# Kernel tuning notes

Hardware: AMD Instinct MI355X
Metric: run time of the kernel (lower is better)

## Reference

```python
import jax, jax.numpy as jnp
import numpy as np

K = 6

def _diag_indices(H, W):
    # stable argsort of anti-diagonal index i+j over row-major flattening
    i = np.arange(H)[:, None]
    j = np.arange(W)[None, :]
    order = np.argsort((i + j).ravel(), kind='stable')
    return order, np.argsort(order, kind='stable')

def _selective_scan(u, delta, A, Bs, Cs, D, delta_bias):
    # u, delta: (B,K,D,L); A: (K,D,N); Bs,Cs: (B,K,N,L); D,delta_bias: (K,D)
    delta = jax.nn.softplus(delta + delta_bias[None, :, :, None])
    dA = jnp.exp(jnp.einsum('bkdl,kdn->lbkdn', delta, A))          # (L,B,K,D,N)
    dBu = jnp.einsum('bkdl,bknl,bkdl->lbkdn', delta, Bs, u)         # (L,B,K,D,N)
    Cl = jnp.moveaxis(Cs, -1, 0)                                    # (L,B,K,N)
    x0 = jnp.zeros(dA.shape[1:], dA.dtype)
    def step(x, inp):
        dA_t, dBu_t, C_t = inp
        x = dA_t * x + dBu_t
        y = jnp.einsum('bkdn,bkn->bkd', x, C_t)
        return x, y
    _, ys = jax.lax.scan(step, x0, (dA, dBu, Cl))
    y = jnp.moveaxis(ys, 0, -1)                                     # (B,K,D,L)
    return y + u * D[None, :, :, None]

def reference(x, W_in, conv_w, conv_b, x_proj_w, dt_w, dt_b, A_logs, Ds, ln_g, ln_b, W_out):
    B, H, W, C = x.shape
    L = H * W
    di = dt_w.shape[1]
    dt_rank = dt_w.shape[2]
    N = A_logs.shape[1]
    # in_proj (no bias) and split
    xz = jnp.einsum('bhwc,oc->bhwo', x, W_in)
    xx, z = jnp.split(xz, 2, axis=-1)
    # depthwise conv 3x3, SAME padding, + bias, SiLU
    xc = jnp.transpose(xx, (0, 3, 1, 2))                            # (B,di,H,W)
    xc = jax.lax.conv_general_dilated(xc, conv_w, (1, 1), 'SAME',
            feature_group_count=di, dimension_numbers=('NCHW', 'OIHW', 'NCHW'))
    xc = jax.nn.silu(xc + conv_b[None, :, None, None])
    # build 6 scan orderings
    x_flat = xc.reshape(B, di, L)
    x_t = jnp.transpose(xc, (0, 1, 3, 2)).reshape(B, di, L)
    x_hwwh = jnp.stack([x_flat, x_t], axis=1)                       # (B,2,di,L)
    xs4 = jnp.concatenate([x_hwwh, x_hwwh[..., ::-1]], axis=1)      # (B,4,di,L)
    x_invhh = jnp.flip(xc, axis=-1).reshape(B, di, L)               # flip W only
    x_hh = jnp.stack([x_flat, x_invhh], axis=1)                     # (B,2,di,L)
    diag_idx, rev_idx = _diag_indices(H, W)
    xs = jnp.concatenate([xs4, x_hh[..., diag_idx]], axis=1)        # (B,6,di,L)
    # projections
    x_dbl = jnp.einsum('bkdl,kcd->bkcl', xs, x_proj_w)
    dts, Bs, Cs = jnp.split(x_dbl, [dt_rank, dt_rank + N], axis=2)
    dts = jnp.einsum('bkrl,kdr->bkdl', dts, dt_w)
    A = -jnp.exp(A_logs).reshape(K, di, N)
    out_y = _selective_scan(xs, dts, A, Bs, Cs, Ds.reshape(K, di), dt_b)
    # undo the 6 orderings
    inv_y = out_y[:, 2:4][..., ::-1]
    wh_y = jnp.transpose(out_y[:, 1].reshape(B, di, W, H), (0, 1, 3, 2)).reshape(B, di, L)
    invwh_y = jnp.transpose(inv_y[:, 1].reshape(B, di, W, H), (0, 1, 3, 2)).reshape(B, di, L)
    transhh = out_y[:, 4:6][..., rev_idx]
    invhh = transhh[:, 1][..., ::-1]
    y = out_y[:, 0] + inv_y[:, 0] + wh_y + invwh_y + transhh[:, 0] + invhh  # (B,di,L)
    y = jnp.transpose(y, (0, 2, 1)).reshape(B, H, W, di)
    # LayerNorm (eps=1e-5)
    mu = y.mean(-1, keepdims=True)
    var = ((y - mu) ** 2).mean(-1, keepdims=True)
    y = (y - mu) * jax.lax.rsqrt(var + 1e-5) * ln_g + ln_b
    y = y * jax.nn.silu(z)
    return jnp.einsum('bhwd,od->bhwo', y, W_out)

def setup_inputs():
    key = jax.random.key(0)
    ks = jax.random.split(key, 8)
    d_model, di, N, dt_rank = 64, 128, 16, 4
    x = jax.random.normal(ks[0], (1, 64, 64, d_model), jnp.float32)
    W_in = jax.random.normal(ks[1], (2 * di, d_model), jnp.float32) * d_model ** -0.5
    conv_w = jax.random.normal(ks[2], (di, 1, 3, 3), jnp.float32) / 3.0
    conv_b = jnp.zeros((di,), jnp.float32)
    x_proj_w = jax.random.normal(ks[3], (K, dt_rank + 2 * N, di), jnp.float32) * di ** -0.5
    s = dt_rank ** -0.5
    dt_w = jax.random.uniform(ks[4], (K, di, dt_rank), jnp.float32, -s, s)
    dt = jnp.exp(jax.random.uniform(ks[5], (K, di), jnp.float32)
                 * (np.log(0.1) - np.log(0.001)) + np.log(0.001))
    dt = jnp.clip(dt, 1e-4)
    dt_b = dt + jnp.log(-jnp.expm1(-dt))
    A_logs = jnp.log(jnp.tile(jnp.arange(1, N + 1, dtype=jnp.float32)[None, :], (K * di, 1)))
    Ds = jnp.ones((K * di,), jnp.float32)
    ln_g = jnp.ones((di,), jnp.float32)
    ln_b = jnp.zeros((di,), jnp.float32)
    W_out = jax.random.normal(ks[6], (d_model, di), jnp.float32) * di ** -0.5
    return {"x": x, "W_in": W_in, "conv_w": conv_w, "conv_b": conv_b,
            "x_proj_w": x_proj_w, "dt_w": dt_w, "dt_b": dt_b, "A_logs": A_logs,
            "Ds": Ds, "ln_g": ln_g, "ln_b": ln_b, "W_out": W_out}
```

## Files before the change

### kernel.cpp

```cpp
#include <hip/hip_runtime.h>
#include <math.h>

#define L    4096
#define DI   128
#define NS   16
#define KK   6
#define CM   64
#define NC   256
#define CH   16

__device__ __forceinline__ float softplus_f(float x){
    return x > 20.f ? x : __logf(1.f + __expf(x));
}
__device__ __forceinline__ float silu_f(float x){
    return x / (1.f + __expf(-x));
}

__device__ __forceinline__ int rankp(int p){
    int h = p >> 6, w = p & 63, s = h + w;
    int imin = s > 63 ? s - 63 : 0;
    int off = (s < 64) ? (s*(s+1))/2 : 4096 - ((127-s)*(128-s))/2;
    return off + (h - imin);
}

__device__ __forceinline__ int perm_in(int k, int l, const int* __restrict__ diag){
    switch(k){
        case 0: return l;
        case 1: return ((l&63)<<6) | (l>>6);
        case 2: return (L-1) - l;
        case 3: { int m = (L-1)-l; return ((m&63)<<6) | (m>>6); }
        case 4: return diag[l];
        default: return diag[l] ^ 63;
    }
}

__global__ __launch_bounds__(256) void k_init(const float* __restrict__ W_in,
                                              const float* __restrict__ W_out,
                                              const float* __restrict__ conv_w,
                                              const float* __restrict__ xpw,
                                              int* __restrict__ diag_idx,
                                              float* __restrict__ WI4,
                                              float* __restrict__ WO4,
                                              float* __restrict__ cwT,
                                              float* __restrict__ PW40){
    int t = blockIdx.x*256 + threadIdx.x;
    diag_idx[rankp(t)] = t;
    {
        int d4 = t >> 8, o = t & 255;
        ((float4*)WI4)[d4*256 + o] = make_float4(
            W_in[(size_t)o*CM + d4*4+0], W_in[(size_t)o*CM + d4*4+1],
            W_in[(size_t)o*CM + d4*4+2], W_in[(size_t)o*CM + d4*4+3]);
    }
    if(t < 2048){
        int d4 = t >> 6, o = t & 63;
        ((float4*)WO4)[d4*64 + o] = make_float4(
            W_out[(size_t)o*DI + d4*4+0], W_out[(size_t)o*DI + d4*4+1],
            W_out[(size_t)o*DI + d4*4+2], W_out[(size_t)o*DI + d4*4+3]);
    }
    if(t < 9*DI){
        int tap = t >> 7, d = t & 127;
        cwT[t] = conv_w[d*9 + tap];
    }
    for(int r = t; r < KK*40*32; r += 4096){
        int k = r / (40*32), rem = r % (40*32);
        int c = rem >> 5, dd4 = rem & 31;
        float4 v = make_float4(0.f, 0.f, 0.f, 0.f);
        if(c < 36) v = ((const float4*)(xpw + ((size_t)k*36 + c)*DI))[dd4];
        ((float4*)PW40)[r] = v;
    }
}

__global__ __launch_bounds__(256) void k_inproj(const float* __restrict__ x,
                                                const float* __restrict__ WI4,
                                                float* __restrict__ xx_t,
                                                float* __restrict__ sz){
    int pb = blockIdx.x * 8;
    int o  = threadIdx.x;
    __shared__ float xr[8][CM];
    if(o < 128) ((float4*)&xr[0][0])[o] = ((const float4*)(x + (size_t)pb*CM))[o];
    float4 w[16];
    const float4* W4 = (const float4*)WI4;
    #pragma unroll
    for(int q=0;q<16;q++) w[q] = W4[q*256 + o];
    __syncthreads();
    float acc[8];
    #pragma unroll
    for(int pi=0;pi<8;pi++) acc[pi] = 0.f;
    #pragma unroll
    for(int q=0;q<16;q++){
        float4 wv = w[q];
        #pragma unroll
        for(int pi=0;pi<8;pi++){
            float4 xv = *((const float4*)&xr[pi][q*4]);
            acc[pi] += wv.x*xv.x + wv.y*xv.y + wv.z*xv.z + wv.w*xv.w;
        }
    }
    #pragma unroll
    for(int pi=0;pi<8;pi++){
        int p = pb + pi;
        if(o < DI) xx_t[(size_t)p*DI + o] = acc[pi];
        else       sz[(size_t)p*DI + (o-DI)] = silu_f(acc[pi]);
    }
}

__global__ __launch_bounds__(256) void k_conv(const float* __restrict__ xx_t,
                                              const float* __restrict__ cwT,
                                              const float* __restrict__ cb,
                                              float* __restrict__ xc_t){
    int idx = blockIdx.x*256 + threadIdx.x;
    int dq = (idx & 31)*4, p = idx >> 5;
    int h = p >> 6, w = p & 63;
    float4 acc = *((const float4*)(cb + dq));
    #pragma unroll
    for(int dh=-1; dh<=1; dh++){
        int hh = h+dh; if(hh < 0 || hh >= 64) continue;
        #pragma unroll
        for(int dw=-1; dw<=1; dw++){
            int ww = w+dw; if(ww < 0 || ww >= 64) continue;
            int tap = (dh+1)*3 + (dw+1);
            float4 xv = *((const float4*)(xx_t + (size_t)(hh*64+ww)*DI + dq));
            float4 wv = *((const float4*)(cwT + tap*DI + dq));
            acc.x += wv.x*xv.x; acc.y += wv.y*xv.y;
            acc.z += wv.z*xv.z; acc.w += wv.w*xv.w;
        }
    }
    *((float4*)(xc_t + (size_t)p*DI + dq)) =
        make_float4(silu_f(acc.x), silu_f(acc.y), silu_f(acc.z), silu_f(acc.w));
}

#define XT_S 132
__global__ __launch_bounds__(256) void k_projscan(const float* __restrict__ xc_t,
                                                  const float* __restrict__ PW40,
                                                  const int* __restrict__ diag,
                                                  const float* __restrict__ dtw,
                                                  const float* __restrict__ dtb,
                                                  const float* __restrict__ A_logs,
                                                  float* __restrict__ dts,
                                                  float* __restrict__ BT,
                                                  float* __restrict__ CT,
                                                  float* __restrict__ apb,
                                                  float* __restrict__ xlb){
    int b = blockIdx.x;
    int k = b % KK, tile = b / KK;
    int l0 = tile * 32;
    int t = threadIdx.x;
    __shared__ float xt[32*XT_S];
    __shared__ float Btl[32*NS];
    __shared__ float dtt[4*32];

    #pragma unroll
    for(int q=0;q<4;q++){
        int lin = q*256 + t;
        int row = lin >> 5, col4 = lin & 31;
        int p = perm_in(k, l0+row, diag);
        float4 v = ((const float4*)(xc_t + (size_t)p*DI))[col4];
        *((float4*)(xt + row*XT_S + col4*4)) = v;
    }
    __syncthreads();

    {
        int l = t & 31, g = t >> 5;
        const float* xr = xt + l*XT_S;
        float acc[5];
        #pragma unroll
        for(int j=0;j<5;j++) acc[j] = 0.f;
        const float4* wbase = (const float4*)PW40 + (size_t)k*40*32;
        for(int dd4=0; dd4<32; dd4++){
            float4 xv = *((const float4*)(xr + dd4*4));
            #pragma unroll
            for(int j=0;j<5;j++){
                float4 wv = wbase[(g*5+j)*32 + dd4];
                acc[j] += wv.x*xv.x + wv.y*xv.y + wv.z*xv.z + wv.w*xv.w;
            }
        }
        #pragma unroll
        for(int j=0;j<5;j++){
            int c = g*5 + j;
            if(c < 4){
                dts[((size_t)k*4 + c)*L + l0 + l] = acc[j];
                dtt[c*32 + l] = acc[j];
            } else if(c < 20){
                BT[((size_t)k*L + l0 + l)*NS + (c-4)] = acc[j];
                Btl[l*NS + (c-4)] = acc[j];
            } else if(c < 36){
                CT[((size_t)k*L + l0 + l)*NS + (c-20)] = acc[j];
            }
        }
    }
    __syncthreads();

    int h = t >> 7, d = t & 127;
    int cc = tile*2 + h;
    float4 w4 = ((const float4*)dtw)[(size_t)k*DI + d];
    float  bb = dtb[k*DI + d];
    float A[NS];
    {
        const float4* ar = (const float4*)(A_logs + ((size_t)k*DI + d)*NS);
        #pragma unroll
        for(int q=0;q<4;q++){
            float4 a4 = ar[q];
            A[q*4+0] = -__expf(a4.x); A[q*4+1] = -__expf(a4.y);
            A[q*4+2] = -__expf(a4.z); A[q*4+3] = -__expf(a4.w);
        }
    }
    float xs[NS], ap[NS];
    #pragma unroll
    for(int n=0;n<NS;n++){ xs[n] = 0.f; ap[n] = 1.f; }
    #pragma unroll
    for(int i=0;i<CH;i++){
        int l = h*CH + i;
        float u = xt[l*XT_S + d];
        float dv = bb + w4.x*dtt[l] + w4.y*dtt[32+l] + w4.z*dtt[64+l] + w4.w*dtt[96+l];
        float delta = softplus_f(dv);
        float du = delta*u;
        const float* Bi = Btl + l*NS;
        #pragma unroll
        for(int n=0;n<NS;n++){
            float da = __expf(delta*A[n]);
            xs[n] = da*xs[n] + du*Bi[n];
            ap[n] *= da;
        }
    }
    int bk = k*NC + cc;
    float* apd = apb + ((size_t)bk*DI + d)*NS;
    float* xld = xlb + ((size_t)bk*DI + d)*NS;
    #pragma unroll
    for(int q=0;q<4;q++){
        ((float4*)apd)[q] = make_float4(ap[q*4],ap[q*4+1],ap[q*4+2],ap[q*4+3]);
        ((float4*)xld)[q] = make_float4(xs[q*4],xs[q*4+1],xs[q*4+2],xs[q*4+3]);
    }
}

__global__ __launch_bounds__(512) void k_comb(float* __restrict__ apb,
                                              const float* __restrict__ xlb){
    int k    = blockIdx.x >> 5;
    int gidx = blockIdx.x & 31;
    int seg  = threadIdx.x >> 6;
    int c    = threadIdx.x & 63;
    int rem  = gidx*64 + c;
    size_t sb = (size_t)k*NC*2048 + (size_t)seg*32*2048 + rem;
    float a[32], xl[32];
    #pragma unroll
    for(int j=0;j<32;j++){
        a[j]  = apb[sb + (size_t)j*2048];
        xl[j] = xlb[sb + (size_t)j*2048];
    }
    float Aag = 1.f, Xag = 0.f;
    #pragma unroll
    for(int j=0;j<32;j++){ Xag = a[j]*Xag + xl[j]; Aag *= a[j]; }
    __shared__ float sA[64][8], sX[64][8];
    sA[c][seg] = Aag; sX[c][seg] = Xag;
    __syncthreads();
    if(threadIdx.x < 64){
        float run = 0.f;
        #pragma unroll
        for(int s=0;s<8;s++){
            float at = sA[c][s], xt = sX[c][s];
            sX[c][s] = run;
            run = at*run + xt;
        }
    }
    __syncthreads();
    float run = sX[c][seg];
    #pragma unroll
    for(int j=0;j<32;j++){
        apb[sb + (size_t)j*2048] = run;
        run = a[j]*run + xl[j];
    }
}

__global__ __launch_bounds__(128) void k_scan2(const float* __restrict__ xc_t,
                                               const float* __restrict__ dts,
                                               const float* __restrict__ BT,
                                               const float* __restrict__ CT,
                                               const float* __restrict__ dtw,
                                               const float* __restrict__ dtb,
                                               const float* __restrict__ A_logs,
                                               const float* __restrict__ Dsv,
                                               const int* __restrict__ diag,
                                               const float* __restrict__ inib,
                                               float* __restrict__ yk){
    int bk = blockIdx.x;
    int k = bk >> 8, cc = bk & (NC-1);
    int d = threadIdx.x;
    int l0 = cc*CH;
    __shared__ float Bt[CH*NS];
    __shared__ float Ct[CH*NS];
    __shared__ float dtt[4*CH];
    __shared__ int   pt[CH];
    if(d < 64){
        ((float4*)Bt)[d] = ((const float4*)(BT + ((size_t)k*L + l0)*NS))[d];
        int r = d>>4, i = d&15;
        dtt[d] = dts[((size_t)k*4 + r)*L + l0 + i];
    } else {
        ((float4*)Ct)[d-64] = ((const float4*)(CT + ((size_t)k*L + l0)*NS))[d-64];
    }
    if(d < CH) pt[d] = perm_in(k, l0+d, diag);
    __syncthreads();
    float u[CH];
    #pragma unroll
    for(int i=0;i<CH;i++) u[i] = xc_t[(size_t)pt[i]*DI + d];
    float4 w4 = ((const float4*)dtw)[(size_t)k*DI + d];
    float  bb = dtb[k*DI + d];
    float  Dv = Dsv[k*DI + d];
    float A[NS];
    {
        const float4* ar = (const float4*)(A_logs + ((size_t)k*DI + d)*NS);
        #pragma unroll
        for(int q=0;q<4;q++){
            float4 a4 = ar[q];
            A[q*4+0] = -__expf(a4.x); A[q*4+1] = -__expf(a4.y);
            A[q*4+2] = -__expf(a4.z); A[q*4+3] = -__expf(a4.w);
        }
    }
    float xv[NS];
    {
        const float4* ir = (const float4*)(inib + ((size_t)bk*DI + d)*NS);
        #pragma unroll
        for(int q=0;q<4;q++){
            float4 v = ir[q];
            xv[q*4+0]=v.x; xv[q*4+1]=v.y; xv[q*4+2]=v.z; xv[q*4+3]=v.w;
        }
    }
    #pragma unroll
    for(int i=0;i<CH;i++){
        float dv = bb + w4.x*dtt[i] + w4.y*dtt[CH+i] + w4.z*dtt[2*CH+i] + w4.w*dtt[3*CH+i];
        float delta = softplus_f(dv);
        float du = delta*u[i];
        const float* Bi = Bt + i*NS;
        const float* Ci = Ct + i*NS;
        float y = 0.f;
        #pragma unroll
        for(int n=0;n<NS;n++){
            float da = __expf(delta*A[n]);
            xv[n] = da*xv[n] + du*Bi[n];
            y += xv[n]*Ci[n];
        }
        yk[((size_t)k*L + l0 + i)*DI + d] = y + u[i]*Dv;
    }
}

__global__ __launch_bounds__(128) void k_out(const float* __restrict__ yk,
                                             const float* __restrict__ sz,
                                             const float* __restrict__ ln_g,
                                             const float* __restrict__ ln_b,
                                             const float* __restrict__ WO4,
                                             float* __restrict__ out){
    int pb = blockIdx.x*4;
    int d = threadIdx.x;
    __shared__ float ms[4][DI];
    __shared__ float red[4][2][2];
    float g = ln_g[d], bc = ln_b[d];
    float yv[4];
    #pragma unroll
    for(int pi=0;pi<4;pi++){
        int p = pb+pi;
        int tp = ((p&63)<<6) | (p>>6);
        float y;
        y  = yk[((size_t)0*L + p)*DI + d];
        y += yk[((size_t)1*L + tp)*DI + d];
        y += yk[((size_t)2*L + (L-1-p))*DI + d];
        y += yk[((size_t)3*L + (L-1-tp))*DI + d];
        y += yk[((size_t)4*L + rankp(p))*DI + d];
        y += yk[((size_t)5*L + rankp(L-1-p))*DI + d];
        yv[pi] = y;
        float s1 = y, s2 = y*y;
        #pragma unroll
        for(int m=1;m<64;m<<=1){ s1 += __shfl_xor(s1,m,64); s2 += __shfl_xor(s2,m,64); }
        if((d&63)==0){ red[pi][d>>6][0] = s1; red[pi][d>>6][1] = s2; }
    }
    __syncthreads();
    #pragma unroll
    for(int pi=0;pi<4;pi++){
        float mu  = (red[pi][0][0]+red[pi][1][0]) * (1.f/DI);
        float var = (red[pi][0][1]+red[pi][1][1]) * (1.f/DI) - mu*mu;
        float yh = (yv[pi]-mu)*rsqrtf(var+1e-5f)*g + bc;
        ms[pi][d] = yh * sz[(size_t)(pb+pi)*DI + d];
    }
    __syncthreads();
    int o = d & 63, w = d >> 6;
    const float4* W4 = (const float4*)WO4;
    float acc[2];
    acc[0] = 0.f; acc[1] = 0.f;
    #pragma unroll 8
    for(int d4=0; d4<32; d4++){
        float4 wv = W4[d4*64 + o];
        #pragma unroll
        for(int q=0;q<2;q++){
            float4 xv = *((const float4*)&ms[w*2+q][d4*4]);
            acc[q] += wv.x*xv.x + wv.y*xv.y + wv.z*xv.z + wv.w*xv.w;
        }
    }
    #pragma unroll
    for(int q=0;q<2;q++)
        out[(size_t)(pb + w*2 + q)*CM + o] = acc[q];
}

extern "C" void kernel_launch(void* const* d_in, const int* in_sizes, int n_in,
                              void* d_out, int out_size, void* d_ws, size_t ws_size,
                              hipStream_t stream) {
    const float* x      = (const float*)d_in[0];
    const float* W_in   = (const float*)d_in[1];
    const float* conv_w = (const float*)d_in[2];
    const float* conv_b = (const float*)d_in[3];
    const float* xpw    = (const float*)d_in[4];
    const float* dtw    = (const float*)d_in[5];
    const float* dtb    = (const float*)d_in[6];
    const float* A_logs = (const float*)d_in[7];
    const float* Dsv    = (const float*)d_in[8];
    const float* ln_g   = (const float*)d_in[9];
    const float* ln_b   = (const float*)d_in[10];
    const float* W_out  = (const float*)d_in[11];
    float* out = (float*)d_out;

    float* ws = (float*)d_ws;
    float* xx_t = ws;
    float* sz   = xx_t + (size_t)L*DI;
    float* xc_t = sz   + (size_t)L*DI;
    float* dts  = xc_t + (size_t)L*DI;
    float* BT   = dts  + (size_t)KK*4*L;
    float* CT   = BT   + (size_t)KK*L*NS;
    float* apb  = CT   + (size_t)KK*L*NS;
    float* xlb  = apb  + (size_t)KK*NC*DI*NS;
    float* yk   = xlb  + (size_t)KK*NC*DI*NS;
    int*   diag = (int*)(yk + (size_t)KK*L*DI);
    float* WI4  = (float*)(diag + L);
    float* WO4  = WI4 + (size_t)16*256*4;
    float* cwT  = WO4 + (size_t)32*64*4;
    float* PW40 = cwT + (size_t)9*DI;

    k_init    <<<L/256, 256, 0, stream>>>(W_in, W_out, conv_w, xpw, diag, WI4, WO4, cwT, PW40);
    k_inproj  <<<L/8, 256, 0, stream>>>(x, WI4, xx_t, sz);
    k_conv    <<<(L*DI/4)/256, 256, 0, stream>>>(xx_t, cwT, conv_b, xc_t);
    k_projscan<<<KK*128, 256, 0, stream>>>(xc_t, PW40, diag, dtw, dtb, A_logs,
                                           dts, BT, CT, apb, xlb);
    k_comb    <<<KK*32, 512, 0, stream>>>(apb, xlb);
    k_scan2   <<<KK*NC, 128, 0, stream>>>(xc_t, dts, BT, CT, dtw, dtb, A_logs, Dsv, diag, apb, yk);
    k_out     <<<L/4, 128, 0, stream>>>(yk, sz, ln_g, ln_b, WO4, out);
}
```

Baseline: 165.3 us.

## Drop init kernel by reading raw weights and computing diagonal permutation inline

Removes the k_init launch that built the diagonal index table and repacked the in-proj, out-proj, conv and x-proj weights. Kernels now read the original weight layouts directly, and the diagonal scan order is computed arithmetically with a sqrt-based inverse rank. Several kernels change shape along the way: the conv goes from float4 per thread to scalar, the x-proj splits its work as 5/4 rows per group with no padding, out-proj weights are held in registers, and k_comb uses more, smaller blocks. This saves a launch and its global traffic, at the cost of strided weight loads and extra ALU work for the inverse rank.

```diff
diff --git a/kernel.cpp b/kernel.cpp
--- a/kernel.cpp
+++ b/kernel.cpp
@@ -23,55 +23,38 @@
     return off + (h - imin);
 }
 
-__device__ __forceinline__ int perm_in(int k, int l, const int* __restrict__ diag){
+__device__ __forceinline__ int invrank(int r){
+    int s, i;
+    if(r < 2080){
+        s = (int)((sqrtf(8.f*(float)r + 1.f) - 1.f) * 0.5f);
+        while(((s+1)*(s+2))/2 <= r) s++;
+        while((s*(s+1))/2 > r) s--;
+        i = r - (s*(s+1))/2;
+    } else {
+        int q = 4096 - r;
+        int u = (int)((sqrtf(8.f*(float)q + 1.f) - 1.f) * 0.5f);
+        while((u*(u+1))/2 < q) u++;
+        while(u > 1 && ((u-1)*u)/2 >= q) u--;
+        s = 127 - u;
+        int off = 4096 - (u*(u+1))/2;
+        i = (s - 63) + (r - off);
+    }
+    return (i << 6) | (s - i);
+}
+
+__device__ __forceinline__ int perm_in(int k, int l){
     switch(k){
         case 0: return l;
         case 1: return ((l&63)<<6) | (l>>6);
         case 2: return (L-1) - l;
         case 3: { int m = (L-1)-l; return ((m&63)<<6) | (m>>6); }
-        case 4: return diag[l];
-        default: return diag[l] ^ 63;
-    }
-}
-
-__global__ __launch_bounds__(256) void k_init(const float* __restrict__ W_in,
-                                              const float* __restrict__ W_out,
-                                              const float* __restrict__ conv_w,
-                                              const float* __restrict__ xpw,
-                                              int* __restrict__ diag_idx,
-                                              float* __restrict__ WI4,
-                                              float* __restrict__ WO4,
-                                              float* __restrict__ cwT,
-                                              float* __restrict__ PW40){
-    int t = blockIdx.x*256 + threadIdx.x;
-    diag_idx[rankp(t)] = t;
-    {
-        int d4 = t >> 8, o = t & 255;
-        ((float4*)WI4)[d4*256 + o] = make_float4(
-            W_in[(size_t)o*CM + d4*4+0], W_in[(size_t)o*CM + d4*4+1],
-            W_in[(size_t)o*CM + d4*4+2], W_in[(size_t)o*CM + d4*4+3]);
-    }
-    if(t < 2048){
-        int d4 = t >> 6, o = t & 63;
-        ((float4*)WO4)[d4*64 + o] = make_float4(
-            W_out[(size_t)o*DI + d4*4+0], W_out[(size_t)o*DI + d4*4+1],
-            W_out[(size_t)o*DI + d4*4+2], W_out[(size_t)o*DI + d4*4+3]);
-    }
-    if(t < 9*DI){
-        int tap = t >> 7, d = t & 127;
-        cwT[t] = conv_w[d*9 + tap];
-    }
-    for(int r = t; r < KK*40*32; r += 4096){
-        int k = r / (40*32), rem = r % (40*32);
-        int c = rem >> 5, dd4 = rem & 31;
-        float4 v = make_float4(0.f, 0.f, 0.f, 0.f);
-        if(c < 36) v = ((const float4*)(xpw + ((size_t)k*36 + c)*DI))[dd4];
-        ((float4*)PW40)[r] = v;
+        case 4: return invrank(l);
+        default: return invrank(l) ^ 63;
     }
 }
 
 __global__ __launch_bounds__(256) void k_inproj(const float* __restrict__ x,
-                                                const float* __restrict__ WI4,
+                                                const float* __restrict__ W_in,
                                                 float* __restrict__ xx_t,
                                                 float* __restrict__ sz){
     int pb = blockIdx.x * 8;
@@ -79,9 +62,9 @@
     __shared__ float xr[8][CM];
     if(o < 128) ((float4*)&xr[0][0])[o] = ((const float4*)(x + (size_t)pb*CM))[o];
     float4 w[16];
-    const float4* W4 = (const float4*)WI4;
-    #pragma unroll
-    for(int q=0;q<16;q++) w[q] = W4[q*256 + o];
+    const float4* wrow = (const float4*)(W_in + (size_t)o*CM);
+    #pragma unroll
+    for(int q=0;q<16;q++) w[q] = wrow[q];
     __syncthreads();
     float acc[8];
     #pragma unroll
@@ -104,34 +87,28 @@
 }
 
 __global__ __launch_bounds__(256) void k_conv(const float* __restrict__ xx_t,
-                                              const float* __restrict__ cwT,
+                                              const float* __restrict__ cw,
                                               const float* __restrict__ cb,
                                               float* __restrict__ xc_t){
     int idx = blockIdx.x*256 + threadIdx.x;
-    int dq = (idx & 31)*4, p = idx >> 5;
+    int d = idx & 127, p = idx >> 7;
     int h = p >> 6, w = p & 63;
-    float4 acc = *((const float4*)(cb + dq));
+    float acc = cb[d];
     #pragma unroll
     for(int dh=-1; dh<=1; dh++){
         int hh = h+dh; if(hh < 0 || hh >= 64) continue;
         #pragma unroll
         for(int dw=-1; dw<=1; dw++){
             int ww = w+dw; if(ww < 0 || ww >= 64) continue;
-            int tap = (dh+1)*3 + (dw+1);
-            float4 xv = *((const float4*)(xx_t + (size_t)(hh*64+ww)*DI + dq));
-            float4 wv = *((const float4*)(cwT + tap*DI + dq));
-            acc.x += wv.x*xv.x; acc.y += wv.y*xv.y;
-            acc.z += wv.z*xv.z; acc.w += wv.w*xv.w;
-        }
-    }
-    *((float4*)(xc_t + (size_t)p*DI + dq)) =
-        make_float4(silu_f(acc.x), silu_f(acc.y), silu_f(acc.z), silu_f(acc.w));
+            acc += cw[d*9 + (dh+1)*3+(dw+1)] * xx_t[(size_t)(hh*64+ww)*DI + d];
+        }
+    }
+    xc_t[idx] = silu_f(acc);
 }
 
 #define XT_S 132
 __global__ __launch_bounds__(256) void k_projscan(const float* __restrict__ xc_t,
-                                                  const float* __restrict__ PW40,
-                                                  const int* __restrict__ diag,
+                                                  const float* __restrict__ xpw,
                                                   const float* __restrict__ dtw,
                                                   const float* __restrict__ dtb,
                                                   const float* __restrict__ A_logs,
@@ -152,7 +129,7 @@
     for(int q=0;q<4;q++){
         int lin = q*256 + t;
         int row = lin >> 5, col4 = lin & 31;
-        int p = perm_in(k, l0+row, diag);
+        int p = perm_in(k, l0+row);
         float4 v = ((const float4*)(xc_t + (size_t)p*DI))[col4];
         *((float4*)(xt + row*XT_S + col4*4)) = v;
     }
@@ -160,30 +137,36 @@
 
     {
         int l = t & 31, g = t >> 5;
+        int cbase = (g < 4) ? 5*g : 20 + 4*(g-4);
+        int cnt   = (g < 4) ? 5 : 4;
         const float* xr = xt + l*XT_S;
         float acc[5];
         #pragma unroll
         for(int j=0;j<5;j++) acc[j] = 0.f;
-        const float4* wbase = (const float4*)PW40 + (size_t)k*40*32;
+        const float4* wbase = (const float4*)(xpw + (size_t)k*36*DI);
         for(int dd4=0; dd4<32; dd4++){
             float4 xv = *((const float4*)(xr + dd4*4));
             #pragma unroll
             for(int j=0;j<5;j++){
-                float4 wv = wbase[(g*5+j)*32 + dd4];
-                acc[j] += wv.x*xv.x + wv.y*xv.y + wv.z*xv.z + wv.w*xv.w;
+                if(j < cnt){
+                    float4 wv = wbase[(cbase+j)*32 + dd4];
+                    acc[j] += wv.x*xv.x + wv.y*xv.y + wv.z*xv.z + wv.w*xv.w;
+                }
             }
         }
         #pragma unroll
         for(int j=0;j<5;j++){
-            int c = g*5 + j;
-            if(c < 4){
-                dts[((size_t)k*4 + c)*L + l0 + l] = acc[j];
-                dtt[c*32 + l] = acc[j];
-            } else if(c < 20){
-                BT[((size_t)k*L + l0 + l)*NS + (c-4)] = acc[j];
-                Btl[l*NS + (c-4)] = acc[j];
-            } else if(c < 36){
-                CT[((size_t)k*L + l0 + l)*NS + (c-20)] = acc[j];
+            if(j < cnt){
+                int c = cbase + j;
+                if(c < 4){
+                    dts[((size_t)k*4 + c)*L + l0 + l] = acc[j];
+                    dtt[c*32 + l] = acc[j];
+                } else if(c < 20){
+                    BT[((size_t)k*L + l0 + l)*NS + (c-4)] = acc[j];
+                    Btl[l*NS + (c-4)] = acc[j];
+                } else {
+                    CT[((size_t)k*L + l0 + l)*NS + (c-20)] = acc[j];
+                }
             }
         }
     }
@@ -231,39 +214,40 @@
     }
 }
 
-__global__ __launch_bounds__(512) void k_comb(float* __restrict__ apb,
+__global__ __launch_bounds__(256) void k_comb(float* __restrict__ apb,
                                               const float* __restrict__ xlb){
-    int k    = blockIdx.x >> 5;
-    int gidx = blockIdx.x & 31;
-    int seg  = threadIdx.x >> 6;
-    int c    = threadIdx.x & 63;
-    int rem  = gidx*64 + c;
-    size_t sb = (size_t)k*NC*2048 + (size_t)seg*32*2048 + rem;
-    float a[32], xl[32];
-    #pragma unroll
-    for(int j=0;j<32;j++){
+    int k    = blockIdx.x >> 7;
+    int gidx = blockIdx.x & 127;
+    int seg  = threadIdx.x >> 4;
+    int c    = threadIdx.x & 15;
+    int rem  = gidx*16 + c;
+    size_t sb = (size_t)k*NC*2048 + (size_t)seg*16*2048 + rem;
+    float a[16], xl[16];
+    #pragma unroll
+    for(int j=0;j<16;j++){
         a[j]  = apb[sb + (size_t)j*2048];
         xl[j] = xlb[sb + (size_t)j*2048];
     }
     float Aag = 1.f, Xag = 0.f;
     #pragma unroll
-    for(int j=0;j<32;j++){ Xag = a[j]*Xag + xl[j]; Aag *= a[j]; }
-    __shared__ float sA[64][8], sX[64][8];
+    for(int j=0;j<16;j++){ Xag = a[j]*Xag + xl[j]; Aag *= a[j]; }
+    __shared__ float sA[16][17], sX[16][17];
     sA[c][seg] = Aag; sX[c][seg] = Xag;
     __syncthreads();
-    if(threadIdx.x < 64){
+    if(threadIdx.x < 16){
+        int cc = threadIdx.x;
         float run = 0.f;
         #pragma unroll
-        for(int s=0;s<8;s++){
-            float at = sA[c][s], xt = sX[c][s];
-            sX[c][s] = run;
+        for(int s=0;s<16;s++){
+            float at = sA[cc][s], xt = sX[cc][s];
+            sX[cc][s] = run;
             run = at*run + xt;
         }
     }
     __syncthreads();
     float run = sX[c][seg];
     #pragma unroll
-    for(int j=0;j<32;j++){
+    for(int j=0;j<16;j++){
         apb[sb + (size_t)j*2048] = run;
         run = a[j]*run + xl[j];
     }
@@ -277,7 +261,6 @@
                                                const float* __restrict__ dtb,
                                                const float* __restrict__ A_logs,
                                                const float* __restrict__ Dsv,
-                                               const int* __restrict__ diag,
                                                const float* __restrict__ inib,
                                                float* __restrict__ yk){
     int bk = blockIdx.x;
@@ -295,7 +278,7 @@
     } else {
         ((float4*)Ct)[d-64] = ((const float4*)(CT + ((size_t)k*L + l0)*NS))[d-64];
     }
-    if(d < CH) pt[d] = perm_in(k, l0+d, diag);
+    if(d < CH) pt[d] = perm_in(k, l0+d);
     __syncthreads();
     float u[CH];
     #pragma unroll
@@ -344,7 +327,7 @@
                                              const float* __restrict__ sz,
                                              const float* __restrict__ ln_g,
                                              const float* __restrict__ ln_b,
-                                             const float* __restrict__ WO4,
+                                             const float* __restrict__ W_out,
                                              float* __restrict__ out){
     int pb = blockIdx.x*4;
     int d = threadIdx.x;
@@ -379,12 +362,15 @@
     }
     __syncthreads();
     int o = d & 63, w = d >> 6;
-    const float4* W4 = (const float4*)WO4;
+    float4 wreg[32];
+    const float4* wr4 = (const float4*)(W_out + (size_t)o*DI);
+    #pragma unroll
+    for(int q=0;q<32;q++) wreg[q] = wr4[q];
     float acc[2];
     acc[0] = 0.f; acc[1] = 0.f;
-    #pragma unroll 8
+    #pragma unroll
     for(int d4=0; d4<32; d4++){
-        float4 wv = W4[d4*64 + o];
+        float4 wv = wreg[d4];
         #pragma unroll
         for(int q=0;q<2;q++){
             float4 xv = *((const float4*)&ms[w*2+q][d4*4]);
@@ -423,18 +409,12 @@
     float* apb  = CT   + (size_t)KK*L*NS;
     float* xlb  = apb  + (size_t)KK*NC*DI*NS;
     float* yk   = xlb  + (size_t)KK*NC*DI*NS;
-    int*   diag = (int*)(yk + (size_t)KK*L*DI);
-    float* WI4  = (float*)(diag + L);
-    float* WO4  = WI4 + (size_t)16*256*4;
-    float* cwT  = WO4 + (size_t)32*64*4;
-    float* PW40 = cwT + (size_t)9*DI;
-
-    k_init    <<<L/256, 256, 0, stream>>>(W_in, W_out, conv_w, xpw, diag, WI4, WO4, cwT, PW40);
-    k_inproj  <<<L/8, 256, 0, stream>>>(x, WI4, xx_t, sz);
-    k_conv    <<<(L*DI/4)/256, 256, 0, stream>>>(xx_t, cwT, conv_b, xc_t);
-    k_projscan<<<KK*128, 256, 0, stream>>>(xc_t, PW40, diag, dtw, dtb, A_logs,
+
+    k_inproj  <<<L/8, 256, 0, stream>>>(x, W_in, xx_t, sz);
+    k_conv    <<<(L*DI)/256, 256, 0, stream>>>(xx_t, conv_w, conv_b, xc_t);
+    k_projscan<<<KK*128, 256, 0, stream>>>(xc_t, xpw, dtw, dtb, A_logs,
                                            dts, BT, CT, apb, xlb);
-    k_comb    <<<KK*32, 512, 0, stream>>>(apb, xlb);
-    k_scan2   <<<KK*NC, 128, 0, stream>>>(xc_t, dts, BT, CT, dtw, dtb, A_logs, Dsv, diag, apb, yk);
-    k_out     <<<L/4, 128, 0, stream>>>(yk, sz, ln_g, ln_b, WO4, out);
-}
+    k_comb    <<<KK*128, 256, 0, stream>>>(apb, xlb);
+    k_scan2   <<<KK*NC, 128, 0, stream>>>(xc_t, dts, BT, CT, dtw, dtb, A_logs, Dsv, apb, yk);
+    k_out     <<<L/4, 128, 0, stream>>>(yk, sz, ln_g, ln_b, W_out, out);
+}
```

Result: slower. 175.8 us (+6.4%).
